# Kernel tuning notes

Measured on AMD Instinct MI355X. Metric: run time of the kernel, lower is better.

Reference implementation:

```python
import jax, jax.numpy as jnp
import numpy as np

B, Q, K, DQ, DK, H, DV = 4, 1024, 1024, 256, 256, 64, 256

def setup_inputs() -> dict:
    key = jax.random.key(0)
    k1, k2, k3, k4, k5, k6 = jax.random.split(key, 6)
    queries = jax.random.normal(k1, (B, Q, DQ), dtype=jnp.float32)
    keys = jax.random.normal(k2, (B, K, DK), dtype=jnp.float32)
    values = jax.random.normal(k3, (B, K, DV), dtype=jnp.float32)
    # learned params (stored as (in, out) so x @ W matches nn.Linear)
    W_q = jax.random.normal(k4, (DQ, H), dtype=jnp.float32) / np.sqrt(DQ)
    W_k = jax.random.normal(k5, (DK, H), dtype=jnp.float32) / np.sqrt(DK)
    w_v = jax.random.normal(k6, (H,), dtype=jnp.float32) / np.sqrt(H)
    return {"queries": queries, "keys": keys, "values": values,
            "W_q": W_q, "W_k": W_k, "w_v": w_v}

def reference(queries, keys, values, W_q, W_k, w_v):
    # projections: [B,Q,H], [B,K,H]
    q = jnp.einsum('bqd,dh->bqh', queries, W_q)
    k = jnp.einsum('bkd,dh->bkh', keys, W_k)
    # broadcast add -> tanh -> reduce with w_v: scores [B,Q,K]
    features = jnp.tanh(q[:, :, None, :] + k[:, None, :, :])  # [B,Q,K,H]
    scores = jnp.einsum('bqkh,h->bqk', features, w_v)
    attn = jax.nn.softmax(scores, axis=-1)  # dropout is identity in eval
    return jnp.einsum('bqk,bkv->bqv', attn, values)
```

## Files before the change

kernel.cpp:

```cpp
#include <hip/hip_runtime.h>

#define Bn 4
#define Qn 1024
#define Kn 1024
#define Dd 256
#define Hh 64
#define Dv 256
#define TQ 16

typedef __attribute__((ext_vector_type(8))) short short8;
typedef __attribute__((ext_vector_type(4))) float floatx4;

__device__ __forceinline__ short f32_to_bf16(float x) {
    unsigned u = __float_as_uint(x);
    unsigned r = u + 0x7fffu + ((u >> 16) & 1u);
    return (short)(r >> 16);
}
__device__ __forceinline__ float bf16_to_f32(short h) {
    return __uint_as_float(((unsigned)(unsigned short)h) << 16);
}

__global__ __launch_bounds__(256) void prep_kernel(const float* __restrict__ Xq,
                                                   const float* __restrict__ Wq,
                                                   const float* __restrict__ Xk,
                                                   const float* __restrict__ Wk,
                                                   const float* __restrict__ V,
                                                   float* __restrict__ Eq,
                                                   float* __restrict__ Ekt,
                                                   short* __restrict__ Vhi,
                                                   short* __restrict__ Vlo) {
    __shared__ float tile[32 * 261];
    int t = threadIdx.x;
    if (blockIdx.x < 512) {
        int gw = blockIdx.x * 4 + (t >> 6);
        int h = t & 63;
        int side = gw >> 10;
        int row0 = (gw & 1023) * 4;
        const float* X = side ? Xk : Xq;
        const float* W = side ? Wk : Wq;
        float acc[4] = {0.f, 0.f, 0.f, 0.f};
        for (int d4 = 0; d4 < Dd / 4; ++d4) {
            float w0 = W[(d4 * 4 + 0) * Hh + h];
            float w1 = W[(d4 * 4 + 1) * Hh + h];
            float w2 = W[(d4 * 4 + 2) * Hh + h];
            float w3 = W[(d4 * 4 + 3) * Hh + h];
            #pragma unroll
            for (int r = 0; r < 4; ++r) {
                float4 xv = ((const float4*)(X + (row0 + r) * Dd))[d4];
                acc[r] = fmaf(xv.x, w0, acc[r]);
                acc[r] = fmaf(xv.y, w1, acc[r]);
                acc[r] = fmaf(xv.z, w2, acc[r]);
                acc[r] = fmaf(xv.w, w3, acc[r]);
            }
        }
        #pragma unroll
        for (int r = 0; r < 4; ++r) {
            int row = row0 + r;
            float e = __expf(2.f * acc[r]);
            if (!side) {
                Eq[row * Hh + h] = e;
            } else {
                int b = row >> 10, k = row & 1023;
                Ekt[(b * Hh + h) * Kn + k] = e;
            }
        }
    } else {
        int blk = blockIdx.x - 512;
        int b = blk >> 5;
        int kt = blk & 31;
        const float* Vg = V + (b * Kn + kt * 32) * Dv;
        for (int i = 0; i < 8; ++i) {
            int k = i * 4 + (t >> 6);
            int n4 = (t & 63) * 4;
            float4 v = *(const float4*)(Vg + k * Dv + n4);
            tile[k * 261 + n4 + 0] = v.x;
            tile[k * 261 + n4 + 1] = v.y;
            tile[k * 261 + n4 + 2] = v.z;
            tile[k * 261 + n4 + 3] = v.w;
        }
        __syncthreads();
        int wave = t >> 6, l = t & 63;
        int n_in = l & 15, kc = l >> 4;
        for (int p = 0; p < 4; ++p) {
            int nt = wave * 4 + p;
            int n = nt * 16 + n_in;
            short8 hi, lo;
            #pragma unroll
            for (int j = 0; j < 8; ++j) {
                float x = tile[(kc * 8 + j) * 261 + n];
                short hs = f32_to_bf16(x);
                hi[j] = hs;
                lo[j] = f32_to_bf16(x - bf16_to_f32(hs));
            }
            size_t base = (((size_t)(b * 32 + kt) * 16 + nt) * 512) + (size_t)l * 8;
            *(short8*)(Vhi + base) = hi;
            *(short8*)(Vlo + base) = lo;
        }
    }
}

__global__ __launch_bounds__(1024, 4) void attn_kernel(const float* __restrict__ Eq,
                                                       const float* __restrict__ Ekt,
                                                       const short* __restrict__ Vhi,
                                                       const short* __restrict__ Vlo,
                                                       const float* __restrict__ wv,
                                                       float* __restrict__ out) {
    __shared__ __align__(16) unsigned sc[TQ * 1028];
    __shared__ float wsum[16 * TQ];
    __shared__ float rinv_s[TQ];

    int tid = threadIdx.x;
    int blk = blockIdx.x;
    int b = (blk & 7) >> 1;
    int tile = (blk >> 3) * 2 + (blk & 1);
    int qbase = tile * TQ;

    const float* kb = Ekt + b * Hh * Kn;
    const float* qp = Eq + (size_t)(b * Qn + qbase) * Hh;
    float s[TQ];
    #pragma unroll
    for (int q = 0; q < TQ; ++q) s[q] = 0.f;

    float e0 = kb[0 * Kn + tid];
    float e1 = kb[1 * Kn + tid];
    float e2 = kb[2 * Kn + tid];
    float e3 = kb[3 * Kn + tid];
    for (int h4 = 0; h4 < Hh / 4; ++h4) {
        float n0, n1, n2, n3;
        if (h4 < Hh / 4 - 1) {
            const float* kn = kb + (h4 + 1) * 4 * Kn;
            n0 = kn[0 * Kn + tid];
            n1 = kn[1 * Kn + tid];
            n2 = kn[2 * Kn + tid];
            n3 = kn[3 * Kn + tid];
        }
        float4 w4 = ((const float4*)wv)[h4];
        #pragma unroll
        for (int q = 0; q < TQ; ++q) {
            float4 qv = *(const float4*)(qp + q * Hh + h4 * 4);
            float a  = fmaf(qv.x, e0, 1.f);
            float bb = fmaf(qv.y, e1, 1.f);
            float c  = fmaf(qv.z, e2, 1.f);
            float d  = fmaf(qv.w, e3, 1.f);
            float nab = fmaf(w4.x, bb, w4.y * a);
            float ncd = fmaf(w4.z, d, w4.w * c);
            s[q] = fmaf(nab, __builtin_amdgcn_rcpf(a * bb), s[q]);
            s[q] = fmaf(ncd, __builtin_amdgcn_rcpf(c * d), s[q]);
        }
        e0 = n0; e1 = n1; e2 = n2; e3 = n3;
    }

    unsigned short* sp = (unsigned short*)sc;
    float part[TQ];
    #pragma unroll
    for (int q = 0; q < TQ; ++q) {
        float p = __expf(-2.f * s[q]);
        part[q] = p;
        short hs = f32_to_bf16(p);
        sp[q * 2056 + tid] = (unsigned short)hs;
        sp[q * 2056 + 1024 + tid] = (unsigned short)f32_to_bf16(p - bf16_to_f32(hs));
    }

    int wave = tid >> 6, lane = tid & 63;
    #pragma unroll
    for (int q = 0; q < TQ; ++q) {
        #pragma unroll
        for (int off = 32; off >= 1; off >>= 1)
            part[q] += __shfl_xor(part[q], off, 64);
    }
    if (lane == 0) {
        #pragma unroll
        for (int q = 0; q < TQ; ++q) wsum[wave * TQ + q] = part[q];
    }
    __syncthreads();

    {
        float v = (lane < 16) ? wsum[lane * TQ + wave] : 0.f;
        v += __shfl_xor(v, 8, 64);
        v += __shfl_xor(v, 4, 64);
        v += __shfl_xor(v, 2, 64);
        v += __shfl_xor(v, 1, 64);
        if (lane == 0) rinv_s[wave] = 1.f / v;
    }
    __syncthreads();

    int qf = lane & 15, kc = lane >> 4;
    floatx4 acc = {0.f, 0.f, 0.f, 0.f};
    const char* scb = (const char*)sc;
    for (int kt = 0; kt < 32; ++kt) {
        short8 bhi = *(const short8*)(scb + qf * 4112 + kt * 64 + kc * 16);
        short8 blo = *(const short8*)(scb + qf * 4112 + 2048 + kt * 64 + kc * 16);
        size_t base = (((size_t)(b * 32 + kt) * 16 + wave) * 512) + (size_t)lane * 8;
        short8 ah = *(const short8*)(Vhi + base);
        short8 al = *(const short8*)(Vlo + base);
        acc = __builtin_amdgcn_mfma_f32_16x16x32_bf16(ah, bhi, acc, 0, 0, 0);
        acc = __builtin_amdgcn_mfma_f32_16x16x32_bf16(al, bhi, acc, 0, 0, 0);
        acc = __builtin_amdgcn_mfma_f32_16x16x32_bf16(ah, blo, acc, 0, 0, 0);
    }
    {
        float r = rinv_s[qf];
        float* ob = out + ((size_t)(b * Qn + qbase + qf)) * Dv + wave * 16 + kc * 4;
        float4 o = { acc[0] * r, acc[1] * r, acc[2] * r, acc[3] * r };
        *(float4*)ob = o;
    }
}

extern "C" void kernel_launch(void* const* d_in, const int* in_sizes, int n_in,
                              void* d_out, int out_size, void* d_ws, size_t ws_size,
                              hipStream_t stream) {
    const float* queries = (const float*)d_in[0];
    const float* keys    = (const float*)d_in[1];
    const float* values  = (const float*)d_in[2];
    const float* W_q     = (const float*)d_in[3];
    const float* W_k     = (const float*)d_in[4];
    const float* w_v     = (const float*)d_in[5];
    float* out = (float*)d_out;

    float* Eq  = (float*)d_ws;
    float* Ekt = Eq + Bn * Qn * Hh;
    short* Vhi = (short*)(Ekt + Bn * Kn * Hh);
    short* Vlo = Vhi + (size_t)Bn * Kn * Dv;

    prep_kernel<<<640, 256, 0, stream>>>(queries, W_q, keys, W_k, values,
                                         Eq, Ekt, Vhi, Vlo);
    attn_kernel<<<Bn * (Qn / TQ), 1024, 0, stream>>>(Eq, Ekt, Vhi, Vlo, w_v, out);
}
```

Measured before the change: 129.5 us.

## Transpose key projection through LDS and hold all key features in registers

The key projection in the prep kernel moves to its own blocks. Each block computes 64 keys and transposes the result through shared memory, so writes to the transposed Ekt buffer are coalesced instead of strided. In the attention kernel each thread loads all 64 key features into registers once, and the loop order becomes query-outer, head-inner. This drops the per-step prefetch and the 16 running score accumulators. It raises register pressure (64 floats) under launch bounds of 1024 threads, which may cause spills or reduce occupancy.

```diff
diff --git a/kernel.cpp b/kernel.cpp
--- a/kernel.cpp
+++ b/kernel.cpp
@@ -31,22 +31,19 @@
                                                    short* __restrict__ Vlo) {
     __shared__ float tile[32 * 261];
     int t = threadIdx.x;
-    if (blockIdx.x < 512) {
+    if (blockIdx.x < 256) {
         int gw = blockIdx.x * 4 + (t >> 6);
         int h = t & 63;
-        int side = gw >> 10;
-        int row0 = (gw & 1023) * 4;
-        const float* X = side ? Xk : Xq;
-        const float* W = side ? Wk : Wq;
+        int row0 = gw * 4;
         float acc[4] = {0.f, 0.f, 0.f, 0.f};
         for (int d4 = 0; d4 < Dd / 4; ++d4) {
-            float w0 = W[(d4 * 4 + 0) * Hh + h];
-            float w1 = W[(d4 * 4 + 1) * Hh + h];
-            float w2 = W[(d4 * 4 + 2) * Hh + h];
-            float w3 = W[(d4 * 4 + 3) * Hh + h];
+            float w0 = Wq[(d4 * 4 + 0) * Hh + h];
+            float w1 = Wq[(d4 * 4 + 1) * Hh + h];
+            float w2 = Wq[(d4 * 4 + 2) * Hh + h];
+            float w3 = Wq[(d4 * 4 + 3) * Hh + h];
             #pragma unroll
             for (int r = 0; r < 4; ++r) {
-                float4 xv = ((const float4*)(X + (row0 + r) * Dd))[d4];
+                float4 xv = ((const float4*)(Xq + (row0 + r) * Dd))[d4];
                 acc[r] = fmaf(xv.x, w0, acc[r]);
                 acc[r] = fmaf(xv.y, w1, acc[r]);
                 acc[r] = fmaf(xv.z, w2, acc[r]);
@@ -54,18 +51,40 @@
             }
         }
         #pragma unroll
-        for (int r = 0; r < 4; ++r) {
-            int row = row0 + r;
-            float e = __expf(2.f * acc[r]);
-            if (!side) {
-                Eq[row * Hh + h] = e;
-            } else {
-                int b = row >> 10, k = row & 1023;
-                Ekt[(b * Hh + h) * Kn + k] = e;
+        for (int r = 0; r < 4; ++r)
+            Eq[(row0 + r) * Hh + h] = __expf(2.f * acc[r]);
+    } else if (blockIdx.x < 320) {
+        int blkk = blockIdx.x - 256;
+        int b = blkk >> 4, k0 = (blkk & 15) * 64;
+        const float* X = Xk + ((size_t)b * Kn + k0) * Dd;
+        int wv_ = t >> 6, h = t & 63;
+        float acc[16];
+        #pragma unroll
+        for (int r = 0; r < 16; ++r) acc[r] = 0.f;
+        for (int d4 = 0; d4 < Dd / 4; ++d4) {
+            float w0 = Wk[(d4 * 4 + 0) * Hh + h];
+            float w1 = Wk[(d4 * 4 + 1) * Hh + h];
+            float w2 = Wk[(d4 * 4 + 2) * Hh + h];
+            float w3 = Wk[(d4 * 4 + 3) * Hh + h];
+            #pragma unroll
+            for (int r = 0; r < 16; ++r) {
+                float4 xv = ((const float4*)(X + (wv_ * 16 + r) * Dd))[d4];
+                acc[r] = fmaf(xv.x, w0, acc[r]);
+                acc[r] = fmaf(xv.y, w1, acc[r]);
+                acc[r] = fmaf(xv.z, w2, acc[r]);
+                acc[r] = fmaf(xv.w, w3, acc[r]);
             }
         }
+        #pragma unroll
+        for (int r = 0; r < 16; ++r)
+            tile[h * 65 + wv_ * 16 + r] = __expf(2.f * acc[r]);
+        __syncthreads();
+        for (int i = 0; i < 16; ++i) {
+            int ho = wv_ * 16 + i;
+            Ekt[((size_t)b * Hh + ho) * Kn + k0 + h] = tile[ho * 65 + h];
+        }
     } else {
-        int blk = blockIdx.x - 512;
+        int blk = blockIdx.x - 320;
         int b = blk >> 5;
         int kt = blk & 31;
         const float* Vg = V + (b * Kn + kt * 32) * Dv;
@@ -115,46 +134,32 @@
     int tile = (blk >> 3) * 2 + (blk & 1);
     int qbase = tile * TQ;
 
-    const float* kb = Ekt + b * Hh * Kn;
+    const float* kb = Ekt + (size_t)b * Hh * Kn + tid;
+    float e[Hh];
+    #pragma unroll
+    for (int h = 0; h < Hh; ++h) e[h] = kb[(size_t)h * Kn];
+
     const float* qp = Eq + (size_t)(b * Qn + qbase) * Hh;
-    float s[TQ];
-    #pragma unroll
-    for (int q = 0; q < TQ; ++q) s[q] = 0.f;
-
-    float e0 = kb[0 * Kn + tid];
-    float e1 = kb[1 * Kn + tid];
-    float e2 = kb[2 * Kn + tid];
-    float e3 = kb[3 * Kn + tid];
-    for (int h4 = 0; h4 < Hh / 4; ++h4) {
-        float n0, n1, n2, n3;
-        if (h4 < Hh / 4 - 1) {
-            const float* kn = kb + (h4 + 1) * 4 * Kn;
-            n0 = kn[0 * Kn + tid];
-            n1 = kn[1 * Kn + tid];
-            n2 = kn[2 * Kn + tid];
-            n3 = kn[3 * Kn + tid];
-        }
-        float4 w4 = ((const float4*)wv)[h4];
-        #pragma unroll
-        for (int q = 0; q < TQ; ++q) {
-            float4 qv = *(const float4*)(qp + q * Hh + h4 * 4);
-            float a  = fmaf(qv.x, e0, 1.f);
-            float bb = fmaf(qv.y, e1, 1.f);
-            float c  = fmaf(qv.z, e2, 1.f);
-            float d  = fmaf(qv.w, e3, 1.f);
+    const float4* wv4 = (const float4*)wv;
+    unsigned short* sp = (unsigned short*)sc;
+    float part[TQ];
+    for (int q = 0; q < TQ; ++q) {
+        const float4* qr = (const float4*)(qp + q * Hh);
+        float s = 0.f;
+        #pragma unroll
+        for (int h4 = 0; h4 < Hh / 4; ++h4) {
+            float4 qv = qr[h4];
+            float4 w4 = wv4[h4];
+            float a  = fmaf(qv.x, e[4 * h4 + 0], 1.f);
+            float bb = fmaf(qv.y, e[4 * h4 + 1], 1.f);
+            float c  = fmaf(qv.z, e[4 * h4 + 2], 1.f);
+            float d  = fmaf(qv.w, e[4 * h4 + 3], 1.f);
             float nab = fmaf(w4.x, bb, w4.y * a);
             float ncd = fmaf(w4.z, d, w4.w * c);
-            s[q] = fmaf(nab, __builtin_amdgcn_rcpf(a * bb), s[q]);
-            s[q] = fmaf(ncd, __builtin_amdgcn_rcpf(c * d), s[q]);
-        }
-        e0 = n0; e1 = n1; e2 = n2; e3 = n3;
-    }
-
-    unsigned short* sp = (unsigned short*)sc;
-    float part[TQ];
-    #pragma unroll
-    for (int q = 0; q < TQ; ++q) {
-        float p = __expf(-2.f * s[q]);
+            s = fmaf(nab, __builtin_amdgcn_rcpf(a * bb), s);
+            s = fmaf(ncd, __builtin_amdgcn_rcpf(c * d), s);
+        }
+        float p = __expf(-2.f * s);
         part[q] = p;
         short hs = f32_to_bf16(p);
         sp[q * 2056 + tid] = (unsigned short)hs;
@@ -221,7 +226,7 @@
     short* Vhi = (short*)(Ekt + Bn * Kn * Hh);
     short* Vlo = Vhi + (size_t)Bn * Kn * Dv;
 
-    prep_kernel<<<640, 256, 0, stream>>>(queries, W_q, keys, W_k, values,
+    prep_kernel<<<448, 256, 0, stream>>>(queries, W_q, keys, W_k, values,
                                          Eq, Ekt, Vhi, Vlo);
     attn_kernel<<<Bn * (Qn / TQ), 1024, 0, stream>>>(Eq, Ekt, Vhi, Vlo, w_v, out);
 }
```

Result: slower. 154.6 us (+19.4%).
